# Kernel tuning notes

Measured on AMD Instinct MI355X. Metric: run time of the kernel, lower is better.

## Reference

```python
import jax, jax.numpy as jnp
import numpy as np

NF, NLOC, NNEI = 4, 2048, 64
EMBED, PAIR_DIM, H = 128, 64, 8
HD = EMBED // H
EPS = 1e-5

def _ln(x, g, b):
    m = x.mean(-1, keepdims=True)
    v = ((x - m) ** 2).mean(-1, keepdims=True)
    return (x - m) * jax.lax.rsqrt(v + EPS) * g + b

def setup_inputs() -> dict:
    key = jax.random.key(0)
    ks = jax.random.split(key, 12)
    inp = {
        "query": jax.random.normal(ks[0], (NF, NLOC, EMBED), jnp.float32),
        "pair": jax.random.normal(ks[1], (NF, NLOC, NNEI, PAIR_DIM), jnp.float32),
        "nlist": jax.random.randint(ks[2], (NF, NLOC, NNEI), 0, NLOC, jnp.int64),
        "delta_pos": jax.random.normal(ks[3], (NF, NLOC, NNEI, 3), jnp.float32),
        "attn_mask": jnp.zeros((NF, H, NLOC, NNEI), jnp.float32),
        "ln_g": jnp.ones((EMBED,), jnp.float32),
        "ln_b": jnp.zeros((EMBED,), jnp.float32),
        "pn_g": jnp.ones((PAIR_DIM,), jnp.float32),
        "pn_b": jnp.zeros((PAIR_DIM,), jnp.float32),
        "Wq": jax.random.normal(ks[4], (EMBED, EMBED), jnp.float32) * (EMBED ** -0.5),
        "Wk": jax.random.normal(ks[5], (EMBED, EMBED), jnp.float32) * (EMBED ** -0.5),
        "Wv": jax.random.normal(ks[6], (EMBED, EMBED), jnp.float32) * (EMBED ** -0.5),
        "Wbias": jax.random.normal(ks[7], (H, PAIR_DIM), jnp.float32) * (PAIR_DIM ** -0.5),
        "bbias": jnp.zeros((H,), jnp.float32),
        "Wforce": jax.random.normal(ks[8], (1, EMBED), jnp.float32) * (EMBED ** -0.5),
    }
    return inp

def reference(query, pair, nlist, delta_pos, attn_mask,
              ln_g, ln_b, pn_g, pn_b, Wq, Wk, Wv, Wbias, bbias, Wforce):
    nf, nloc, _ = query.shape
    nnei = nlist.shape[-1]
    qn = _ln(query, ln_g, ln_b)            # [f,l,e]
    pn = _ln(pair, pn_g, pn_b)             # [f,l,n,p]
    scaling = HD ** -0.5
    q = (qn @ Wq.T).reshape(nf, nloc, H, HD) * scaling       # [f,l,h,d]
    k = qn @ Wk.T                                            # [f,l,e]
    v = qn @ Wv.T
    idx = nlist.reshape(nf, -1)[..., None]                   # [f,l*n,1]
    kg = jnp.take_along_axis(k, idx, axis=1).reshape(nf, nloc, nnei, H, HD)
    vg = jnp.take_along_axis(v, idx, axis=1).reshape(nf, nloc, nnei, H, HD)
    attn = jnp.einsum('flhd,flnhd->fhln', q, kg)             # [f,h,l,n]
    bias = jnp.einsum('flnp,hp->fhln', pn, Wbias) + bbias[None, :, None, None]
    probs = jax.nn.softmax(attn + attn_mask + bias, axis=-1)  # dropout off (eval)
    # rotate by delta_pos and contract with v over neighbors
    x = jnp.einsum('fhln,flnc,flnhd->flchd', probs, delta_pos, vg)
    x = x.reshape(nf, nloc, 3, EMBED)
    force = (x @ Wforce.T).squeeze(-1)                       # [f,l,3]
    return force
```

## Files before the change

kernel.cpp:

```cpp
#include <hip/hip_runtime.h>

#define NFR   4
#define NLOCC 2048
#define NNEIN 64
#define EMB   128
#define PDIM  64
#define NH    8
#define LNEPS 1e-5f
#define NROW  (NFR*NLOCC)

#define WS_Q   0
#define WS_K   (NROW*EMB)
#define WS_FV  (2*NROW*EMB)

__device__ __forceinline__ void fma4(float4& acc, const float4 a, const float4 b) {
    acc.x = fmaf(a.x, b.x, acc.x);
    acc.y = fmaf(a.y, b.y, acc.y);
    acc.z = fmaf(a.z, b.z, acc.z);
    acc.w = fmaf(a.w, b.w, acc.w);
}
__device__ __forceinline__ void fma4s(float4& acc, const float s, const float4 b) {
    acc.x = fmaf(s, b.x, acc.x);
    acc.y = fmaf(s, b.y, acc.y);
    acc.z = fmaf(s, b.z, acc.z);
    acc.w = fmaf(s, b.w, acc.w);
}
__device__ __forceinline__ float hsum4(const float4 a) {
    return (a.x + a.y) + (a.z + a.w);
}
__device__ __forceinline__ float dot4(const float4 a, const float4 b) {
    return fmaf(a.x, b.x, fmaf(a.y, b.y, fmaf(a.z, b.z, a.w * b.w)));
}
__device__ __forceinline__ float4 scale4(const float4 a, const float s) {
    return make_float4(a.x*s, a.y*s, a.z*s, a.w*s);
}

__global__ __launch_bounds__(256, 2) void qkfv_kernel(
    const float* __restrict__ query,
    const float* __restrict__ ln_g, const float* __restrict__ ln_b,
    const float* __restrict__ Wq, const float* __restrict__ Wk,
    const float* __restrict__ Wv, const float* __restrict__ Wforce,
    float* __restrict__ ws)
{
    __shared__ float  gb_s[2][EMB];
    __shared__ float  qn_s[16*132];
    __shared__ float  wt_s[2][16*132];
    __shared__ float4 wvf_s4[8*33];
    const int t = threadIdx.x;
    const int rowbase = blockIdx.x * 16;

    if (t < 64) {
        const float* src = (t < 32) ? ln_g : ln_b;
        ((float4*)gb_s[t >> 5])[t & 31] = ((const float4*)src)[t & 31];
    }

    {
        const int h = t >> 5, ch = t & 31;
        float4 acc = make_float4(0.f, 0.f, 0.f, 0.f);
        #pragma unroll
        for (int d = 0; d < 16; ++d) {
            const float wf = Wforce[h*16 + d];
            const float4 wv = ((const float4*)(Wv + (size_t)(h*16 + d)*EMB))[ch];
            fma4s(acc, wf, wv);
        }
        wvf_s4[h*33 + ch] = acc;
    }

    const int r   = t >> 4;
    const int seg = t & 15;
    float4 x0 = ((const float4*)query)[(size_t)(rowbase + r)*32 + seg*2 + 0];
    float4 x1 = ((const float4*)query)[(size_t)(rowbase + r)*32 + seg*2 + 1];
    float s  = (x0.x + x0.y) + (x0.z + x0.w) + (x1.x + x1.y) + (x1.z + x1.w);
    float ss = x0.x*x0.x + x0.y*x0.y + x0.z*x0.z + x0.w*x0.w
             + x1.x*x1.x + x1.y*x1.y + x1.z*x1.z + x1.w*x1.w;
    #pragma unroll
    for (int m = 1; m < 16; m <<= 1) {
        s  += __shfl_xor(s,  m, 64);
        ss += __shfl_xor(ss, m, 64);
    }
    const float mean = s * (1.0f / 128.0f);
    const float var  = ss * (1.0f / 128.0f) - mean * mean;
    const float rstd = rsqrtf(var + LNEPS);
    __syncthreads();

    {
        const int c0 = seg * 8;
        float4 o0, o1;
        o0.x = (x0.x - mean)*rstd*gb_s[0][c0+0] + gb_s[1][c0+0];
        o0.y = (x0.y - mean)*rstd*gb_s[0][c0+1] + gb_s[1][c0+1];
        o0.z = (x0.z - mean)*rstd*gb_s[0][c0+2] + gb_s[1][c0+2];
        o0.w = (x0.w - mean)*rstd*gb_s[0][c0+3] + gb_s[1][c0+3];
        o1.x = (x1.x - mean)*rstd*gb_s[0][c0+4] + gb_s[1][c0+4];
        o1.y = (x1.y - mean)*rstd*gb_s[0][c0+5] + gb_s[1][c0+5];
        o1.z = (x1.z - mean)*rstd*gb_s[0][c0+6] + gb_s[1][c0+6];
        o1.w = (x1.w - mean)*rstd*gb_s[0][c0+7] + gb_s[1][c0+7];
        ((float4*)qn_s)[r*33 + seg*2 + 0] = o0;
        ((float4*)qn_s)[r*33 + seg*2 + 1] = o1;
    }
    __syncthreads();

    const int rp = t >> 5;
    const int r0 = rp * 2;
    const int cq = t & 31;
    const int sc0 = t >> 2;
    const int si0 = t & 3;
    const float4* qn4 = (const float4*)qn_s;

    for (int w = 0; w < 2; ++w) {
        const float4* W4 = (const float4*)((w == 0) ? Wq : Wk);
        float4 acc0 = make_float4(0.f,0.f,0.f,0.f);
        float4 acc1 = make_float4(0.f,0.f,0.f,0.f);
        {
            float4 g0 = W4[(size_t)sc0*32 + si0];
            float4 g1 = W4[(size_t)(sc0+64)*32 + si0];
            float* wt = wt_s[0];
            wt[(si0*4+0)*132 + sc0] = g0.x; wt[(si0*4+1)*132 + sc0] = g0.y;
            wt[(si0*4+2)*132 + sc0] = g0.z; wt[(si0*4+3)*132 + sc0] = g0.w;
            wt[(si0*4+0)*132 + sc0+64] = g1.x; wt[(si0*4+1)*132 + sc0+64] = g1.y;
            wt[(si0*4+2)*132 + sc0+64] = g1.z; wt[(si0*4+3)*132 + sc0+64] = g1.w;
        }
        __syncthreads();
        #pragma unroll
        for (int tau = 0; tau < 8; ++tau) {
            const int buf = tau & 1;
            float4 ng0, ng1;
            if (tau < 7) {
                ng0 = W4[(size_t)sc0*32 + (tau+1)*4 + si0];
                ng1 = W4[(size_t)(sc0+64)*32 + (tau+1)*4 + si0];
            }
            const float4* wt4 = (const float4*)wt_s[buf];
            #pragma unroll
            for (int e4 = 0; e4 < 4; ++e4) {
                float4 a0 = qn4[r0*33 + tau*4 + e4];
                float4 a1 = qn4[(r0+1)*33 + tau*4 + e4];
                const float* a0p = (const float*)&a0;
                const float* a1p = (const float*)&a1;
                #pragma unroll
                for (int ee = 0; ee < 4; ++ee) {
                    const float4 wv = wt4[(e4*4+ee)*33 + cq];
                    fma4s(acc0, a0p[ee], wv);
                    fma4s(acc1, a1p[ee], wv);
                }
            }
            if (tau < 7) {
                float* wt = wt_s[buf ^ 1];
                wt[(si0*4+0)*132 + sc0] = ng0.x; wt[(si0*4+1)*132 + sc0] = ng0.y;
                wt[(si0*4+2)*132 + sc0] = ng0.z; wt[(si0*4+3)*132 + sc0] = ng0.w;
                wt[(si0*4+0)*132 + sc0+64] = ng1.x; wt[(si0*4+1)*132 + sc0+64] = ng1.y;
                wt[(si0*4+2)*132 + sc0+64] = ng1.z; wt[(si0*4+3)*132 + sc0+64] = ng1.w;
            }
            __syncthreads();
        }
        const float sc = (w == 0) ? 0.25f : 1.0f;
        float4* dst = (float4*)(ws + (w == 0 ? WS_Q : WS_K));
        dst[(size_t)(rowbase + r0)*32 + cq]     = scale4(acc0, sc);
        dst[(size_t)(rowbase + r0 + 1)*32 + cq] = scale4(acc1, sc);
    }

    if (t < 128) {
        const int rr = t >> 3, h = t & 7;
        float4 acc = make_float4(0.f,0.f,0.f,0.f);
        #pragma unroll
        for (int ch = 0; ch < 32; ++ch)
            fma4(acc, qn4[rr*33 + ch], wvf_s4[h*33 + ch]);
        ws[WS_FV + (size_t)(rowbase + rr)*NH + h] = hsum4(acc);
    }
}

__global__ __launch_bounds__(256, 4) void attn_force_kernel(
    const float* __restrict__ pair, const int* __restrict__ nlist,
    const float* __restrict__ delta_pos, const float* __restrict__ attn_mask,
    const float* __restrict__ pn_g, const float* __restrict__ pn_b,
    const float* __restrict__ Wbias, const float* __restrict__ bbias,
    const float* __restrict__ ws, float* __restrict__ out)
{
    __shared__ float4 pair_s4[64*17];
    __shared__ float  logit_s[NNEIN*9];
    __shared__ float4 G_s4[128];
    __shared__ float  csg_s[16];
    __shared__ float  fv_s[NNEIN*9];
    __shared__ float  dp_s[192];
    __shared__ float  fpart[4][3];

    const int t    = threadIdx.x;
    const int bid  = blockIdx.x;
    const int fr   = bid >> 11;
    const int l    = bid & 2047;
    const int w    = t >> 6;
    const int lane = t & 63;
    const int half = lane >> 5;
    const int c    = lane & 31;
    const int n    = t >> 2;
    const int sub  = t & 3;
    const int h0   = sub * 2, h1 = h0 + 1;
    const int i32  = lane & 31;
    const int hh   = t >> 5;

    {
        const float4* p4 = (const float4*)pair + (size_t)bid*1024;
        #pragma unroll
        for (int i = 0; i < 4; ++i) {
            const int ci   = i*256 + t;
            const float4 v = p4[ci];
            pair_s4[(ci >> 4)*17 + (ci & 15)] = v;
        }
    }
    const int jv = nlist[(size_t)bid*NNEIN + lane];
    const float4 q4c = ((const float4*)(ws + WS_Q))[(size_t)bid*32 + c];

    const float mask0 = attn_mask[((size_t)(fr*NH + h0)*NLOCC + l)*NNEIN + n];
    const float mask1 = attn_mask[((size_t)(fr*NH + h1)*NLOCC + l)*NNEIN + n];

    if (t < 128) {
        const int p4i = t & 15;
        const float4 wb4 = ((const float4*)Wbias)[t];
        const float4 pg4 = ((const float4*)pn_g)[p4i];
        G_s4[t] = make_float4(wb4.x*pg4.x, wb4.y*pg4.y, wb4.z*pg4.z, wb4.w*pg4.w);
    } else if (t < 192) {
        const int h = (t - 128) >> 3, s8 = (t - 128) & 7;
        float sg = 0.f, cb = 0.f;
        #pragma unroll
        for (int k = 0; k < 8; ++k) {
            const int p = s8*8 + k;
            const float wb = Wbias[h*PDIM + p];
            sg = fmaf(pn_g[p], wb, sg);
            cb = fmaf(pn_b[p], wb, cb);
        }
        sg += __shfl_xor(sg, 1, 64); sg += __shfl_xor(sg, 2, 64); sg += __shfl_xor(sg, 4, 64);
        cb += __shfl_xor(cb, 1, 64); cb += __shfl_xor(cb, 2, 64); cb += __shfl_xor(cb, 4, 64);
        if (s8 == 0) { csg_s[h] = sg; csg_s[8 + h] = cb + bbias[h]; }
    } else if (t < 240) {
        ((float4*)dp_s)[t - 192] = ((const float4*)(delta_pos + (size_t)bid*192))[t - 192];
    }

    {
        const int    jn  = __shfl(jv, n & 63, 64);
        const float2 fv2 = ((const float2*)(ws + WS_FV + ((size_t)(fr << 11) + jn)*NH))[sub];
        fv_s[n*9 + h0] = fv2.x;
        fv_s[n*9 + h1] = fv2.y;
    }

    {
        const float4* k4 = (const float4*)(ws + WS_K) + (size_t)(fr << 11)*32;
        int jr[8];
        #pragma unroll
        for (int i = 0; i < 8; ++i)
            jr[i] = __shfl(jv, (w << 4) | (i << 1) | half, 64);
        float4 kkA[4], kkB[4];
        #pragma unroll
        for (int i = 0; i < 4; ++i) kkA[i] = k4[(size_t)jr[i]*32 + c];
        #pragma unroll
        for (int i = 0; i < 4; ++i) kkB[i] = k4[(size_t)jr[4+i]*32 + c];
        float p[8];
        #pragma unroll
        for (int i = 0; i < 4; ++i) p[i]     = dot4(kkA[i], q4c);
        #pragma unroll
        for (int i = 0; i < 4; ++i) p[4 + i] = dot4(kkB[i], q4c);
        #pragma unroll
        for (int i = 0; i < 8; ++i) {
            float pp = p[i];
            pp += __shfl_xor(pp, 1, 64);
            pp += __shfl_xor(pp, 2, 64);
            if ((c & 3) == 0)
                logit_s[((w << 4) | (i << 1) | half)*9 + (c >> 2)] = pp;
        }
    }
    __syncthreads();

    {
        const float4 pr0 = pair_s4[n*17 + sub*4 + 0];
        const float4 pr1 = pair_s4[n*17 + sub*4 + 1];
        const float4 pr2 = pair_s4[n*17 + sub*4 + 2];
        const float4 pr3 = pair_s4[n*17 + sub*4 + 3];
        float s  = hsum4(pr0) + hsum4(pr1) + hsum4(pr2) + hsum4(pr3);
        float ss = dot4(pr0, pr0) + dot4(pr1, pr1) + dot4(pr2, pr2) + dot4(pr3, pr3);
        s  += __shfl_xor(s, 1, 64);  s  += __shfl_xor(s, 2, 64);
        ss += __shfl_xor(ss, 1, 64); ss += __shfl_xor(ss, 2, 64);
        const float mean = s * (1.0f / 64.0f);
        const float var  = ss * (1.0f / 64.0f) - mean * mean;
        const float rstd = rsqrtf(var + LNEPS);

        float d[NH];
        #pragma unroll
        for (int h = 0; h < NH; ++h) d[h] = 0.f;
        const float4 prq[4] = {pr0, pr1, pr2, pr3};
        #pragma unroll
        for (int q = 0; q < 4; ++q) {
            #pragma unroll
            for (int h = 0; h < NH; ++h)
                d[h] += dot4(prq[q], G_s4[h*16 + sub*4 + q]);
        }
        #pragma unroll
        for (int h = 0; h < NH; ++h) {
            d[h] += __shfl_xor(d[h], 1, 64);
            d[h] += __shfl_xor(d[h], 2, 64);
        }
        logit_s[n*9 + h0] += rstd*(d[h0] - mean*csg_s[h0]) + csg_s[8 + h0] + mask0;
        logit_s[n*9 + h1] += rstd*(d[h1] - mean*csg_s[h1]) + csg_s[8 + h1] + mask1;
    }
    __syncthreads();

    {
        const float a = logit_s[i32*9 + hh], b = logit_s[(i32 + 32)*9 + hh];
        float m = fmaxf(a, b);
        #pragma unroll
        for (int mm = 16; mm >= 1; mm >>= 1) m = fmaxf(m, __shfl_xor(m, mm, 64));
        const float ea = __expf(a - m), eb = __expf(b - m);
        float sum = ea + eb;
        #pragma unroll
        for (int mm = 16; mm >= 1; mm >>= 1) sum += __shfl_xor(sum, mm, 64);
        const float inv = 1.0f / sum;
        float ca = ea * inv * fv_s[i32*9 + hh];
        float cb = eb * inv * fv_s[(i32 + 32)*9 + hh];
        ca += __shfl_xor(ca, 32, 64);
        cb += __shfl_xor(cb, 32, 64);
        const float dpax = dp_s[i32*3 + 0],        dpay = dp_s[i32*3 + 1],        dpaz = dp_s[i32*3 + 2];
        const float dpbx = dp_s[(i32+32)*3 + 0],   dpby = dp_s[(i32+32)*3 + 1],   dpbz = dp_s[(i32+32)*3 + 2];
        float f0 = ca*dpax + cb*dpbx;
        float f1 = ca*dpay + cb*dpby;
        float f2 = ca*dpaz + cb*dpbz;
        #pragma unroll
        for (int mm = 1; mm <= 16; mm <<= 1) {
            f0 += __shfl_xor(f0, mm, 64);
            f1 += __shfl_xor(f1, mm, 64);
            f2 += __shfl_xor(f2, mm, 64);
        }
        if (lane == 0) {
            fpart[w][0] = f0; fpart[w][1] = f1; fpart[w][2] = f2;
        }
    }
    __syncthreads();

    if (t < 3)
        out[(size_t)bid*3 + t] = fpart[0][t] + fpart[1][t] + fpart[2][t] + fpart[3][t];
}

extern "C" void kernel_launch(void* const* d_in, const int* in_sizes, int n_in,
                              void* d_out, int out_size, void* d_ws, size_t ws_size,
                              hipStream_t stream) {
    const float* query     = (const float*)d_in[0];
    const float* pair      = (const float*)d_in[1];
    const int*   nlist     = (const int*)d_in[2];
    const float* delta_pos = (const float*)d_in[3];
    const float* attn_mask = (const float*)d_in[4];
    const float* ln_g      = (const float*)d_in[5];
    const float* ln_b      = (const float*)d_in[6];
    const float* pn_g      = (const float*)d_in[7];
    const float* pn_b      = (const float*)d_in[8];
    const float* Wq        = (const float*)d_in[9];
    const float* Wk        = (const float*)d_in[10];
    const float* Wv        = (const float*)d_in[11];
    const float* Wbias     = (const float*)d_in[12];
    const float* bbias     = (const float*)d_in[13];
    const float* Wforce    = (const float*)d_in[14];
    float* out = (float*)d_out;
    float* ws  = (float*)d_ws;

    qkfv_kernel<<<512, 256, 0, stream>>>(query, ln_g, ln_b, Wq, Wk, Wv, Wforce, ws);
    attn_force_kernel<<<NROW, 256, 0, stream>>>(pair, nlist, delta_pos, attn_mask,
                                                pn_g, pn_b, Wbias, bbias, ws, out);
}
```

Baseline: 253.5 us.

## Load pair rows into registers and replicate bias weights per wave to drop a barrier

Each thread now reads its four pair float4s straight from global memory into registers instead of staging the whole pair tile in shared memory. The folded bias weights (G and csg) are computed redundantly by every wave into per-wave shared copies, so the pair-bias phase needs no block-wide barrier after the key gather. The launch-bounds occupancy hint rises from 4 to 6 blocks. The aim is to cut shared-memory traffic and footprint and one __syncthreads; the cost is redundant per-wave weight setup and possibly more register pressure under the tighter bound.

```diff
diff --git a/kernel.cpp b/kernel.cpp
--- a/kernel.cpp
+++ b/kernel.cpp
@@ -167,17 +167,16 @@
     }
 }
 
-__global__ __launch_bounds__(256, 4) void attn_force_kernel(
+__global__ __launch_bounds__(256, 6) void attn_force_kernel(
     const float* __restrict__ pair, const int* __restrict__ nlist,
     const float* __restrict__ delta_pos, const float* __restrict__ attn_mask,
     const float* __restrict__ pn_g, const float* __restrict__ pn_b,
     const float* __restrict__ Wbias, const float* __restrict__ bbias,
     const float* __restrict__ ws, float* __restrict__ out)
 {
-    __shared__ float4 pair_s4[64*17];
     __shared__ float  logit_s[NNEIN*9];
-    __shared__ float4 G_s4[128];
-    __shared__ float  csg_s[16];
+    __shared__ float4 G_s4[4][128];
+    __shared__ float  csg_s[4][16];
     __shared__ float  fv_s[NNEIN*9];
     __shared__ float  dp_s[192];
     __shared__ float  fpart[4][3];
@@ -196,42 +195,46 @@
     const int i32  = lane & 31;
     const int hh   = t >> 5;
 
-    {
-        const float4* p4 = (const float4*)pair + (size_t)bid*1024;
-        #pragma unroll
-        for (int i = 0; i < 4; ++i) {
-            const int ci   = i*256 + t;
-            const float4 v = p4[ci];
-            pair_s4[(ci >> 4)*17 + (ci & 15)] = v;
-        }
-    }
+    const float4* prow = (const float4*)(pair + ((size_t)bid*NNEIN + n)*PDIM);
+    float4 pr0 = prow[sub*4 + 0];
+    float4 pr1 = prow[sub*4 + 1];
+    float4 pr2 = prow[sub*4 + 2];
+    float4 pr3 = prow[sub*4 + 3];
+
     const int jv = nlist[(size_t)bid*NNEIN + lane];
     const float4 q4c = ((const float4*)(ws + WS_Q))[(size_t)bid*32 + c];
 
     const float mask0 = attn_mask[((size_t)(fr*NH + h0)*NLOCC + l)*NNEIN + n];
     const float mask1 = attn_mask[((size_t)(fr*NH + h1)*NLOCC + l)*NNEIN + n];
 
-    if (t < 128) {
-        const int p4i = t & 15;
-        const float4 wb4 = ((const float4*)Wbias)[t];
-        const float4 pg4 = ((const float4*)pn_g)[p4i];
-        G_s4[t] = make_float4(wb4.x*pg4.x, wb4.y*pg4.y, wb4.z*pg4.z, wb4.w*pg4.w);
-    } else if (t < 192) {
-        const int h = (t - 128) >> 3, s8 = (t - 128) & 7;
-        float sg = 0.f, cb = 0.f;
-        #pragma unroll
-        for (int k = 0; k < 8; ++k) {
-            const int p = s8*8 + k;
-            const float wb = Wbias[h*PDIM + p];
-            sg = fmaf(pn_g[p], wb, sg);
-            cb = fmaf(pn_b[p], wb, cb);
-        }
+    {
+        const float4* wb4 = (const float4*)Wbias;
+        const float4* pg4 = (const float4*)pn_g;
+        #pragma unroll
+        for (int i = 0; i < 2; ++i) {
+            const int idx = i*64 + lane;
+            const float4 wb = wb4[idx];
+            const float4 pg = pg4[idx & 15];
+            G_s4[w][idx] = make_float4(wb.x*pg.x, wb.y*pg.y, wb.z*pg.z, wb.w*pg.w);
+        }
+        const int h8 = lane >> 3, s8 = lane & 7;
+        const float4 wba = wb4[h8*16 + s8*2 + 0];
+        const float4 wbb = wb4[h8*16 + s8*2 + 1];
+        const float4 pga = pg4[s8*2 + 0];
+        const float4 pgb = pg4[s8*2 + 1];
+        const float4 pba = ((const float4*)pn_b)[s8*2 + 0];
+        const float4 pbb = ((const float4*)pn_b)[s8*2 + 1];
+        float sg = dot4(wba, pga) + dot4(wbb, pgb);
+        float cb = dot4(wba, pba) + dot4(wbb, pbb);
         sg += __shfl_xor(sg, 1, 64); sg += __shfl_xor(sg, 2, 64); sg += __shfl_xor(sg, 4, 64);
         cb += __shfl_xor(cb, 1, 64); cb += __shfl_xor(cb, 2, 64); cb += __shfl_xor(cb, 4, 64);
-        if (s8 == 0) { csg_s[h] = sg; csg_s[8 + h] = cb + bbias[h]; }
-    } else if (t < 240) {
+        if (s8 == 0) {
+            csg_s[w][h8]     = sg;
+            csg_s[w][8 + h8] = cb + bbias[h8];
+        }
+    }
+    if (t >= 192 && t < 240)
         ((float4*)dp_s)[t - 192] = ((const float4*)(delta_pos + (size_t)bid*192))[t - 192];
-    }
 
     {
         const int    jn  = __shfl(jv, n & 63, 64);
@@ -265,13 +268,8 @@
                 logit_s[((w << 4) | (i << 1) | half)*9 + (c >> 2)] = pp;
         }
     }
-    __syncthreads();
-
-    {
-        const float4 pr0 = pair_s4[n*17 + sub*4 + 0];
-        const float4 pr1 = pair_s4[n*17 + sub*4 + 1];
-        const float4 pr2 = pair_s4[n*17 + sub*4 + 2];
-        const float4 pr3 = pair_s4[n*17 + sub*4 + 3];
+
+    {
         float s  = hsum4(pr0) + hsum4(pr1) + hsum4(pr2) + hsum4(pr3);
         float ss = dot4(pr0, pr0) + dot4(pr1, pr1) + dot4(pr2, pr2) + dot4(pr3, pr3);
         s  += __shfl_xor(s, 1, 64);  s  += __shfl_xor(s, 2, 64);
@@ -288,15 +286,15 @@
         for (int q = 0; q < 4; ++q) {
             #pragma unroll
             for (int h = 0; h < NH; ++h)
-                d[h] += dot4(prq[q], G_s4[h*16 + sub*4 + q]);
+                d[h] += dot4(prq[q], G_s4[w][h*16 + sub*4 + q]);
         }
         #pragma unroll
         for (int h = 0; h < NH; ++h) {
             d[h] += __shfl_xor(d[h], 1, 64);
             d[h] += __shfl_xor(d[h], 2, 64);
         }
-        logit_s[n*9 + h0] += rstd*(d[h0] - mean*csg_s[h0]) + csg_s[8 + h0] + mask0;
-        logit_s[n*9 + h1] += rstd*(d[h1] - mean*csg_s[h1]) + csg_s[8 + h1] + mask1;
+        logit_s[n*9 + h0] += rstd*(d[h0] - mean*csg_s[w][h0]) + csg_s[w][8 + h0] + mask0;
+        logit_s[n*9 + h1] += rstd*(d[h1] - mean*csg_s[w][h1]) + csg_s[w][8 + h1] + mask1;
     }
     __syncthreads();
 
@@ -314,8 +312,8 @@
         float cb = eb * inv * fv_s[(i32 + 32)*9 + hh];
         ca += __shfl_xor(ca, 32, 64);
         cb += __shfl_xor(cb, 32, 64);
-        const float dpax = dp_s[i32*3 + 0],        dpay = dp_s[i32*3 + 1],        dpaz = dp_s[i32*3 + 2];
-        const float dpbx = dp_s[(i32+32)*3 + 0],   dpby = dp_s[(i32+32)*3 + 1],   dpbz = dp_s[(i32+32)*3 + 2];
+        const float dpax = dp_s[i32*3 + 0],      dpay = dp_s[i32*3 + 1],      dpaz = dp_s[i32*3 + 2];
+        const float dpbx = dp_s[(i32+32)*3 + 0], dpby = dp_s[(i32+32)*3 + 1], dpbz = dp_s[(i32+32)*3 + 2];
         float f0 = ca*dpax + cb*dpbx;
         float f1 = ca*dpay + cb*dpby;
         float f2 = ca*dpaz + cb*dpbz;
```

Result: no change. 258.3 us (+1.9%).
